# Performance work log

Hardware: AMD Instinct MI355X
Metric: run time of the kernel (lower is better)

The kernel has to match this reference:

```python
import jax, jax.numpy as jnp
import numpy as np

N = 50000      # num nodes
E = 600000     # num edges (avg degree 12)
IN = 256       # in_feats
H = 128        # h_feats
P = 2          # prop_step
LN_EPS = 1e-5


def setup_inputs() -> dict:
    key = jax.random.key(0)
    ks = jax.random.split(key, 8)
    return {
        "in_feat": jax.random.normal(ks[0], (N, IN), jnp.float32),
        "row": jax.random.randint(ks[1], (E,), 0, N),  # target node of each edge
        "col": jax.random.randint(ks[2], (E,), 0, N),  # source node of each edge
        "lin_w": jax.random.normal(ks[3], (H, IN), jnp.float32) / np.sqrt(IN).astype(np.float32),
        "lin_b": jnp.zeros((H,), jnp.float32),
        "conv_w": jax.random.normal(ks[4], (H, H), jnp.float32) / np.sqrt(H).astype(np.float32),
        "conv_b": jnp.zeros((H,), jnp.float32),
        "root_emb": jax.random.normal(ks[5], (1, H), jnp.float32) * 0.02,
        "ln_gamma": jnp.ones((P, H), jnp.float32),
        "ln_beta": jnp.zeros((P, H), jnp.float32),
    }


def _layernorm(x, g, b):
    mu = jnp.mean(x, axis=-1, keepdims=True)
    var = jnp.mean(jnp.square(x - mu), axis=-1, keepdims=True)
    return (x - mu) * jax.lax.rsqrt(var + LN_EPS) * g + b


def reference(in_feat, row, col, lin_w, lin_b, conv_w, conv_b, root_emb, ln_gamma, ln_beta):
    n = in_feat.shape[0]
    h = in_feat @ lin_w.T + lin_b                      # [N, H]

    # OGB-style degree norm with +1 trick (original edges, row = target)
    deg = jax.ops.segment_sum(jnp.ones_like(row, dtype=h.dtype), row, num_segments=n) + 1.0
    deg_inv = 1.0 / deg                                # deg >= 1, never inf

    # GCNConv symmetric norm with self loops: D^-1/2 (A+I) D^-1/2
    loop = jnp.arange(n)
    r2 = jnp.concatenate([row, loop])                  # [E+N] targets
    c2 = jnp.concatenate([col, loop])                  # [E+N] sources
    d2 = jax.ops.segment_sum(jnp.ones_like(r2, dtype=h.dtype), r2, num_segments=n)
    dis = jnp.where(d2 > 0, jax.lax.rsqrt(jnp.maximum(d2, 1.0)), 0.0)
    ew = dis[r2] * dis[c2]                             # [E+N] edge weights

    root = root_emb[0]                                 # [H]
    ori = h
    for i in range(P):
        if i != 0:
            h = h + ori                                # residual
            h = _layernorm(h, ln_gamma[i], ln_beta[i])
            h = jax.nn.relu(h)
            # dropout=0.0 -> identity
        xw = h @ conv_w.T                              # [N, H]
        h_msg = jax.ops.segment_sum(ew[:, None] * xw[c2], r2, num_segments=n) + conv_b
        root_contrib = jax.nn.relu(h + root) * deg_inv[:, None]
        h = h_msg + root_contrib
    return h
```

## Files before the change

kernel.cpp:

```cpp
#include <hip/hip_runtime.h>
#include <stdint.h>

#define NN 50000
#define EE 600000
#define INF 256
#define HF 128
#define CEB ((EE + 255) / 256)
#define GBT ((NN + 63) / 64)
#define NT0 500
#define NT1 (GBT - NT0)
#define NBCH ((NN + 255) / 256)

typedef __attribute__((ext_vector_type(8))) short short8;
typedef __attribute__((ext_vector_type(4))) float floatx4;

__device__ __forceinline__ unsigned short f32_to_bf16_rne(float x) {
    unsigned int u = __float_as_uint(x);
    unsigned int r = (u + 0x7FFFu + ((u >> 16) & 1u)) >> 16;
    return (unsigned short)r;
}
__device__ __forceinline__ float bf16_to_f32(unsigned short h) {
    return __uint_as_float(((unsigned int)h) << 16);
}
__device__ __forceinline__ float bf16lo_u32(unsigned int u) {
    return __uint_as_float(u << 16);
}
__device__ __forceinline__ float bf16hi_u32(unsigned int u) {
    return __uint_as_float(u & 0xFFFF0000u);
}
__device__ __forceinline__ void cvt_hilo8(float4 v0, float4 v1, short8& hs, short8& ls) {
    float x[8] = {v0.x, v0.y, v0.z, v0.w, v1.x, v1.y, v1.z, v1.w};
    union { short8 s; unsigned short u[8]; } H, L;
#pragma unroll
    for (int k = 0; k < 8; ++k) {
        unsigned short hi = f32_to_bf16_rne(x[k]);
        H.u[k] = hi;
        L.u[k] = f32_to_bf16_rne(x[k] - bf16_to_f32(hi));
    }
    hs = H.s;
    ls = L.s;
}

__device__ __forceinline__ void prepack_one(int idx, const float* lw, const float* cw,
                                            unsigned short* fl, unsigned short* fc) {
    const float* src; unsigned short* dst; int K, c;
    if (idx < 8192) { src = lw; dst = fl; K = INF; c = idx; }
    else            { src = cw; dst = fc; K = HF; c = idx - 8192; }
    int lane = c & 63;
    int nt = (c >> 6) & 7;
    int hl = (c >> 9) & 1;
    int kc = c >> 10;
    int rw = nt * 16 + (lane & 15);
    int koff = kc * 32 + (lane >> 4) * 8;
    const float* p = &src[(size_t)rw * K + koff];
    float4 v0 = *reinterpret_cast<const float4*>(p);
    float4 v1 = *reinterpret_cast<const float4*>(p + 4);
    short8 hs, ls;
    cvt_hilo8(v0, v1, hs, ls);
    *reinterpret_cast<short8*>(&dst[(size_t)c * 8]) = hl ? ls : hs;
}

__global__ void zero_prepack(const float* __restrict__ lw, const float* __restrict__ cw,
                             unsigned short* __restrict__ fl, unsigned short* __restrict__ fc,
                             int* __restrict__ cnt, int* __restrict__ done_ctr) {
    int g = blockIdx.x * 256 + threadIdx.x;
    if (g < 12288) prepack_one(g, lw, cw, fl, fc);
    for (int i = g; i < NN; i += 256 * 256) cnt[i] = 0;
    if (g == 0) *done_ctr = 0;
}

__global__ void scan_all(const int* __restrict__ cnt, int* __restrict__ bsum,
                         int* __restrict__ done_ctr, int* __restrict__ row_start,
                         float* __restrict__ deg_inv, float* __restrict__ dis) {
    __shared__ int sdata[256];
    __shared__ int eb[256];
    __shared__ int flag;
    int c = blockIdx.x, t = threadIdx.x;
    int i = c * 256 + t;
    int v = (i < NN) ? cnt[i] : 0;
    sdata[t] = v;
    __syncthreads();
    for (int s = 1; s < 256; s <<= 1) {
        int add = (t >= s) ? sdata[t - s] : 0;
        __syncthreads();
        sdata[t] += add;
        __syncthreads();
    }
    if (i < NN) {
        row_start[i] = sdata[t] - v;
        float d = (float)(v + 1);
        deg_inv[i] = 1.0f / d;
        dis[i] = rsqrtf(d);
    }
    if (t == 255) bsum[c] = sdata[255];
    __syncthreads();
    if (t == 0) {
        __threadfence();
        flag = (atomicAdd(done_ctr, 1) == NBCH - 1);
    }
    __syncthreads();
    if (!flag) return;
    __threadfence();
    int bv = (t < NBCH) ? bsum[t] : 0;
    sdata[t] = bv;
    __syncthreads();
    for (int s = 1; s < 256; s <<= 1) {
        int add = (t >= s) ? sdata[t - s] : 0;
        __syncthreads();
        sdata[t] += add;
        __syncthreads();
    }
    eb[t] = sdata[t] - bv;
    __syncthreads();
    for (int j = t; j < NN; j += 256) row_start[j] += eb[j >> 8];
    if (t == 0) row_start[NN] = EE;
}

template <int K, int MODE>
__device__ __forceinline__ void gemm_tile(
    int bidx,
    const float* __restrict__ Af,
    const unsigned short* __restrict__ Ahg, const unsigned short* __restrict__ Alg,
    const unsigned short* __restrict__ Wf,
    const float* __restrict__ bias,
    float* __restrict__ C, unsigned short* __restrict__ Cbf,
    const float* __restrict__ h, const float* __restrict__ deg_inv,
    const float* __restrict__ root,
    const float* __restrict__ gamma, const float* __restrict__ beta,
    unsigned short* WS, int M) {
    constexpr int NKC = K / 32;
    const int t = threadIdx.x;
    const int wave = t >> 6;
    const int lane = t & 63;
    const int lrow = lane & 15;
    const int quad = lane >> 4;
    const int bm = bidx * 64;
    int arow = bm + wave * 16 + lrow;
    if (arow >= M) arow = M - 1;

    floatx4 acc[8];
#pragma unroll
    for (int nt = 0; nt < 8; ++nt) acc[nt] = (floatx4){0.f, 0.f, 0.f, 0.f};

#pragma unroll
    for (int pp = 0; pp < NKC / 2; ++pp) {
        if (pp) __syncthreads();
        {
            const unsigned short* src = Wf + (size_t)pp * 16384 + (size_t)t * 8;
#if __has_builtin(__builtin_amdgcn_global_load_lds)
#pragma unroll
            for (int i = 0; i < 8; ++i) {
                __builtin_amdgcn_global_load_lds(
                    (const unsigned int*)(src + (size_t)i * 2048),
                    (unsigned int*)(WS + ((size_t)i * 256 + (t >> 6) * 64) * 8),
                    16, 0, 0);
            }
#else
            const uint4* s4 = reinterpret_cast<const uint4*>(Wf + (size_t)pp * 16384);
            uint4* d4 = reinterpret_cast<uint4*>(WS);
#pragma unroll
            for (int i = 0; i < 8; ++i) d4[t + 256 * i] = s4[t + 256 * i];
#endif
        }
        __syncthreads();
#pragma unroll
        for (int k2 = 0; k2 < 2; ++k2) {
            int kc = pp * 2 + k2;
            short8 afh, afl;
            if (MODE == 0) {
                const float* ap = &Af[(size_t)arow * K + kc * 32 + quad * 8];
                float4 a0 = *reinterpret_cast<const float4*>(ap);
                float4 a1 = *reinterpret_cast<const float4*>(ap + 4);
                cvt_hilo8(a0, a1, afh, afl);
            } else {
                size_t ao = (size_t)arow * K + kc * 32 + quad * 8;
                afh = *reinterpret_cast<const short8*>(&Ahg[ao]);
                afl = *reinterpret_cast<const short8*>(&Alg[ao]);
            }
            const unsigned short* wb = &WS[k2 * 8192 + lane * 8];
#pragma unroll
            for (int nt = 0; nt < 8; ++nt) {
                short8 bfh = *reinterpret_cast<const short8*>(wb + nt * 512);
                short8 bfl = *reinterpret_cast<const short8*>(wb + 4096 + nt * 512);
                acc[nt] = __builtin_amdgcn_mfma_f32_16x16x32_bf16(afh, bfh, acc[nt], 0, 0, 0);
                acc[nt] = __builtin_amdgcn_mfma_f32_16x16x32_bf16(afl, bfh, acc[nt], 0, 0, 0);
                acc[nt] = __builtin_amdgcn_mfma_f32_16x16x32_bf16(afh, bfl, acc[nt], 0, 0, 0);
            }
        }
    }

    float cb[8], rt[8], gm[8], bt[8];
#pragma unroll
    for (int nt = 0; nt < 8; ++nt) {
        int colh = nt * 16 + lrow;
        cb[nt] = bias[colh];
        if (MODE >= 1) rt[nt] = root[colh];
        if (MODE == 1) { gm[nt] = gamma[colh]; bt[nt] = beta[colh]; }
    }

#pragma unroll
    for (int r = 0; r < 4; ++r) {
        int grow = bm + wave * 16 + quad * 4 + r;
        bool ok = (grow < M);
        int gr = ok ? grow : M - 1;
        float x[8];
        if (MODE == 0) {
#pragma unroll
            for (int nt = 0; nt < 8; ++nt) x[nt] = acc[nt][r] + cb[nt];
        } else {
            float di = deg_inv[gr];
            float hv[8];
#pragma unroll
            for (int nt = 0; nt < 8; ++nt) hv[nt] = h[(size_t)gr * HF + nt * 16 + lrow];
#pragma unroll
            for (int nt = 0; nt < 8; ++nt) {
                float v = acc[nt][r] + cb[nt] + fmaxf(hv[nt] + rt[nt], 0.f) * di;
                x[nt] = (MODE == 1) ? v + hv[nt] : v;
            }
        }
        if (MODE == 1) {
            float s = 0.f;
#pragma unroll
            for (int nt = 0; nt < 8; ++nt) s += x[nt];
#pragma unroll
            for (int m = 1; m < 16; m <<= 1) s += __shfl_xor(s, m, 64);
            float mu = s * (1.0f / HF);
            float var = 0.f;
#pragma unroll
            for (int nt = 0; nt < 8; ++nt) { float d = x[nt] - mu; var += d * d; }
#pragma unroll
            for (int m = 1; m < 16; m <<= 1) var += __shfl_xor(var, m, 64);
            float rs = rsqrtf(var * (1.0f / HF) + 1e-5f);
            if (ok) {
#pragma unroll
                for (int nt = 0; nt < 8; ++nt) {
                    int colh = nt * 16 + lrow;
                    float y = fmaxf((x[nt] - mu) * rs * gm[nt] + bt[nt], 0.f);
                    C[(size_t)grow * HF + colh] = y;
                    Cbf[(size_t)grow * HF + colh] = f32_to_bf16_rne(y);
                }
            }
        } else if (MODE == 0) {
            if (ok) {
#pragma unroll
                for (int nt = 0; nt < 8; ++nt) {
                    int colh = nt * 16 + lrow;
                    C[(size_t)grow * HF + colh] = x[nt];
                    Cbf[(size_t)grow * HF + colh] = f32_to_bf16_rne(x[nt]);
                }
            }
        } else {
            if (ok) {
#pragma unroll
                for (int nt = 0; nt < 8; ++nt)
                    C[(size_t)grow * HF + nt * 16 + lrow] = x[nt];
            }
        }
    }
}

__global__ __launch_bounds__(256) void gemm0_count(
    const float* __restrict__ in_feat, const unsigned short* __restrict__ fl,
    const float* __restrict__ lin_b,
    float* __restrict__ h0, unsigned short* __restrict__ hbf,
    const int* __restrict__ row, int* __restrict__ cnt, int* __restrict__ pos) {
    __shared__ unsigned short WS[2 * 8192];
    int b = blockIdx.x;
    if (b < NT0) {
        gemm_tile<INF, 0>(b, in_feat, nullptr, nullptr, fl, lin_b,
                          h0, hbf, nullptr, nullptr, nullptr,
                          nullptr, nullptr, WS, NN);
        return;
    }
    int e = (b - NT0) * 256 + threadIdx.x;
    if (e < EE) pos[e] = atomicAdd(&cnt[row[e]], 1);
}

__global__ __launch_bounds__(256) void gemm0_fill(
    const float* __restrict__ in_feat, const unsigned short* __restrict__ fl,
    const float* __restrict__ lin_b,
    float* __restrict__ h0, unsigned short* __restrict__ hbf,
    const int* __restrict__ row, const int* __restrict__ col,
    const int* __restrict__ row_start, const int* __restrict__ pos,
    int* __restrict__ csr_col) {
    __shared__ unsigned short WS[2 * 8192];
    int b = blockIdx.x;
    if (b < NT1) {
        gemm_tile<INF, 0>(NT0 + b, in_feat, nullptr, nullptr, fl, lin_b,
                          h0, hbf, nullptr, nullptr, nullptr,
                          nullptr, nullptr, WS, NN);
        return;
    }
    int e = (b - NT1) * 256 + threadIdx.x;
    if (e < EE) {
        int p = row_start[row[e]] + pos[e];
        __builtin_nontemporal_store(col[e], &csr_col[p]);
    }
}

template <int MODE>
__global__ __launch_bounds__(256) void gemm_conv(
    const unsigned short* __restrict__ agg_hi, const unsigned short* __restrict__ agg_lo,
    const unsigned short* __restrict__ fc, const float* __restrict__ conv_b,
    float* __restrict__ C, unsigned short* __restrict__ Cbf,
    const float* __restrict__ h, const float* __restrict__ deg_inv,
    const float* __restrict__ root,
    const float* __restrict__ gamma, const float* __restrict__ beta) {
    __shared__ unsigned short WS[2 * 8192];
    gemm_tile<HF, MODE>(blockIdx.x, nullptr, agg_hi, agg_lo, fc, conv_b,
                        C, Cbf, h, deg_inv, root, gamma, beta, WS, NN);
}

__global__ void aggregate(const int* __restrict__ row_start, const int* __restrict__ csr_col,
                          const float* __restrict__ dis, const float* __restrict__ deg_inv,
                          const float* __restrict__ h, const unsigned short* __restrict__ hbf,
                          unsigned short* __restrict__ agg_hi, unsigned short* __restrict__ agg_lo,
                          int n) {
    int wid = (blockIdx.x * blockDim.x + threadIdx.x) >> 6;
    int lane = threadIdx.x & 63;
    if (wid >= n) return;
    int q = lane >> 4;
    int l16 = lane & 15;
    int s = row_start[wid];
    int e = row_start[wid + 1];
    float a0 = 0.f, a1 = 0.f, a2 = 0.f, a3 = 0.f, a4 = 0.f, a5 = 0.f, a6 = 0.f, a7 = 0.f;
    if (e - s <= 16) {
        int j0 = s + q;
        bool p0 = j0 < e, p1 = j0 + 4 < e, p2 = j0 + 8 < e, p3 = j0 + 12 < e;
        int c0 = p0 ? csr_col[j0] : 0;
        int c1 = p1 ? csr_col[j0 + 4] : 0;
        int c2 = p2 ? csr_col[j0 + 8] : 0;
        int c3 = p3 ? csr_col[j0 + 12] : 0;
        float d0 = dis[c0], d1 = dis[c1], d2 = dis[c2], d3 = dis[c3];
        uint4 z = make_uint4(0, 0, 0, 0);
        uint4 g0 = z, g1 = z, g2 = z, g3 = z;
        if (p0) g0 = *reinterpret_cast<const uint4*>(&hbf[(size_t)c0 * HF + l16 * 8]);
        if (p1) g1 = *reinterpret_cast<const uint4*>(&hbf[(size_t)c1 * HF + l16 * 8]);
        if (p2) g2 = *reinterpret_cast<const uint4*>(&hbf[(size_t)c2 * HF + l16 * 8]);
        if (p3) g3 = *reinterpret_cast<const uint4*>(&hbf[(size_t)c3 * HF + l16 * 8]);
        a0 = d0 * bf16lo_u32(g0.x) + d1 * bf16lo_u32(g1.x) + d2 * bf16lo_u32(g2.x) + d3 * bf16lo_u32(g3.x);
        a1 = d0 * bf16hi_u32(g0.x) + d1 * bf16hi_u32(g1.x) + d2 * bf16hi_u32(g2.x) + d3 * bf16hi_u32(g3.x);
        a2 = d0 * bf16lo_u32(g0.y) + d1 * bf16lo_u32(g1.y) + d2 * bf16lo_u32(g2.y) + d3 * bf16lo_u32(g3.y);
        a3 = d0 * bf16hi_u32(g0.y) + d1 * bf16hi_u32(g1.y) + d2 * bf16hi_u32(g2.y) + d3 * bf16hi_u32(g3.y);
        a4 = d0 * bf16lo_u32(g0.z) + d1 * bf16lo_u32(g1.z) + d2 * bf16lo_u32(g2.z) + d3 * bf16lo_u32(g3.z);
        a5 = d0 * bf16hi_u32(g0.z) + d1 * bf16hi_u32(g1.z) + d2 * bf16hi_u32(g2.z) + d3 * bf16hi_u32(g3.z);
        a6 = d0 * bf16lo_u32(g0.w) + d1 * bf16lo_u32(g1.w) + d2 * bf16lo_u32(g2.w) + d3 * bf16lo_u32(g3.w);
        a7 = d0 * bf16hi_u32(g0.w) + d1 * bf16hi_u32(g1.w) + d2 * bf16hi_u32(g2.w) + d3 * bf16hi_u32(g3.w);
    } else {
        float b0 = 0.f, b1 = 0.f, b2 = 0.f, b3 = 0.f, b4 = 0.f, b5 = 0.f, b6 = 0.f, b7 = 0.f;
        int j = s + q;
        for (; j + 4 < e; j += 8) {
            int c0 = csr_col[j];
            int c1 = csr_col[j + 4];
            float d0 = dis[c0];
            float d1 = dis[c1];
            uint4 h0 = *reinterpret_cast<const uint4*>(&hbf[(size_t)c0 * HF + l16 * 8]);
            uint4 h1 = *reinterpret_cast<const uint4*>(&hbf[(size_t)c1 * HF + l16 * 8]);
            a0 = fmaf(d0, bf16lo_u32(h0.x), a0); a1 = fmaf(d0, bf16hi_u32(h0.x), a1);
            a2 = fmaf(d0, bf16lo_u32(h0.y), a2); a3 = fmaf(d0, bf16hi_u32(h0.y), a3);
            a4 = fmaf(d0, bf16lo_u32(h0.z), a4); a5 = fmaf(d0, bf16hi_u32(h0.z), a5);
            a6 = fmaf(d0, bf16lo_u32(h0.w), a6); a7 = fmaf(d0, bf16hi_u32(h0.w), a7);
            b0 = fmaf(d1, bf16lo_u32(h1.x), b0); b1 = fmaf(d1, bf16hi_u32(h1.x), b1);
            b2 = fmaf(d1, bf16lo_u32(h1.y), b2); b3 = fmaf(d1, bf16hi_u32(h1.y), b3);
            b4 = fmaf(d1, bf16lo_u32(h1.z), b4); b5 = fmaf(d1, bf16hi_u32(h1.z), b5);
            b6 = fmaf(d1, bf16lo_u32(h1.w), b6); b7 = fmaf(d1, bf16hi_u32(h1.w), b7);
        }
        if (j < e) {
            int c0 = csr_col[j];
            float d0 = dis[c0];
            uint4 h0 = *reinterpret_cast<const uint4*>(&hbf[(size_t)c0 * HF + l16 * 8]);
            a0 = fmaf(d0, bf16lo_u32(h0.x), a0); a1 = fmaf(d0, bf16hi_u32(h0.x), a1);
            a2 = fmaf(d0, bf16lo_u32(h0.y), a2); a3 = fmaf(d0, bf16hi_u32(h0.y), a3);
            a4 = fmaf(d0, bf16lo_u32(h0.z), a4); a5 = fmaf(d0, bf16hi_u32(h0.z), a5);
            a6 = fmaf(d0, bf16lo_u32(h0.w), a6); a7 = fmaf(d0, bf16hi_u32(h0.w), a7);
        }
        a0 += b0; a1 += b1; a2 += b2; a3 += b3;
        a4 += b4; a5 += b5; a6 += b6; a7 += b7;
    }
#pragma unroll
    for (int m = 16; m < 64; m <<= 1) {
        a0 += __shfl_xor(a0, m, 64);
        a1 += __shfl_xor(a1, m, 64);
        a2 += __shfl_xor(a2, m, 64);
        a3 += __shfl_xor(a3, m, 64);
        a4 += __shfl_xor(a4, m, 64);
        a5 += __shfl_xor(a5, m, 64);
        a6 += __shfl_xor(a6, m, 64);
        a7 += __shfl_xor(a7, m, 64);
    }
    if (q == 0) {
        float dn = dis[wid];
        float di = deg_inv[wid];
        float4 hA = *reinterpret_cast<const float4*>(&h[(size_t)wid * HF + l16 * 8]);
        float4 hB = *reinterpret_cast<const float4*>(&h[(size_t)wid * HF + l16 * 8 + 4]);
        float o[8];
        o[0] = fmaf(dn, a0, di * hA.x);
        o[1] = fmaf(dn, a1, di * hA.y);
        o[2] = fmaf(dn, a2, di * hA.z);
        o[3] = fmaf(dn, a3, di * hA.w);
        o[4] = fmaf(dn, a4, di * hB.x);
        o[5] = fmaf(dn, a5, di * hB.y);
        o[6] = fmaf(dn, a6, di * hB.z);
        o[7] = fmaf(dn, a7, di * hB.w);
        unsigned short hi[8], lo[8];
#pragma unroll
        for (int k = 0; k < 8; ++k) {
            hi[k] = f32_to_bf16_rne(o[k]);
            lo[k] = f32_to_bf16_rne(o[k] - bf16_to_f32(hi[k]));
        }
        uint4 hp, lp;
        hp.x = (unsigned)hi[0] | ((unsigned)hi[1] << 16);
        hp.y = (unsigned)hi[2] | ((unsigned)hi[3] << 16);
        hp.z = (unsigned)hi[4] | ((unsigned)hi[5] << 16);
        hp.w = (unsigned)hi[6] | ((unsigned)hi[7] << 16);
        lp.x = (unsigned)lo[0] | ((unsigned)lo[1] << 16);
        lp.y = (unsigned)lo[2] | ((unsigned)lo[3] << 16);
        lp.z = (unsigned)lo[4] | ((unsigned)lo[5] << 16);
        lp.w = (unsigned)lo[6] | ((unsigned)lo[7] << 16);
        *reinterpret_cast<uint4*>(&agg_hi[(size_t)wid * HF + l16 * 8]) = hp;
        *reinterpret_cast<uint4*>(&agg_lo[(size_t)wid * HF + l16 * 8]) = lp;
    }
}

extern "C" void kernel_launch(void* const* d_in, const int* in_sizes, int n_in,
                              void* d_out, int out_size, void* d_ws, size_t ws_size,
                              hipStream_t stream) {
    const int N = NN;
    const float* in_feat = (const float*)d_in[0];
    const int* row = (const int*)d_in[1];
    const int* col = (const int*)d_in[2];
    const float* lin_w = (const float*)d_in[3];
    const float* lin_b = (const float*)d_in[4];
    const float* conv_w = (const float*)d_in[5];
    const float* conv_b = (const float*)d_in[6];
    const float* root_emb = (const float*)d_in[7];
    const float* ln_gamma = (const float*)d_in[8];
    const float* ln_beta = (const float*)d_in[9];
    float* out = (float*)d_out;

    float* ws = (float*)d_ws;
    size_t o = 0;
    float* deg_inv = ws + o; o += N;
    float* dis = ws + o; o += N;
    int* cnt = (int*)(ws + o); o += N;
    int* row_start = (int*)(ws + o); o += N + 4;
    int* pos = (int*)(ws + o); o += EE;
    int* bsum = (int*)(ws + o); o += 256;
    int* done_ctr = (int*)(ws + o); o += 4;
    int* csr_col = (int*)(ws + o); o += EE;
    unsigned short* fl = (unsigned short*)(ws + o); o += 32768;
    unsigned short* fc = (unsigned short*)(ws + o); o += 16384;
    float* h0 = ws + o; o += (size_t)N * HF;
    unsigned short* hbf = (unsigned short*)(ws + o); o += (size_t)N * HF / 2;
    unsigned short* agg_hi = (unsigned short*)(ws + o); o += (size_t)N * HF / 2;
    unsigned short* agg_lo = (unsigned short*)(ws + o); o += (size_t)N * HF / 2;

    const int WB = (N + 3) / 4;

    zero_prepack<<<256, 256, 0, stream>>>(lin_w, conv_w, fl, fc, cnt, done_ctr);
    gemm0_count<<<NT0 + CEB, 256, 0, stream>>>(in_feat, fl, lin_b, h0, hbf, row, cnt, pos);
    scan_all<<<NBCH, 256, 0, stream>>>(cnt, bsum, done_ctr, row_start, deg_inv, dis);
    gemm0_fill<<<NT1 + CEB, 256, 0, stream>>>(in_feat, fl, lin_b, h0, hbf,
                                              row, col, row_start, pos, csr_col);

    aggregate<<<WB, 256, 0, stream>>>(row_start, csr_col, dis, deg_inv, h0, hbf,
                                      agg_hi, agg_lo, N);
    gemm_conv<1><<<GBT, 256, 0, stream>>>(agg_hi, agg_lo, fc, conv_b, h0, hbf,
                                          h0, deg_inv, root_emb,
                                          ln_gamma + HF, ln_beta + HF);

    aggregate<<<WB, 256, 0, stream>>>(row_start, csr_col, dis, deg_inv, h0, hbf,
                                      agg_hi, agg_lo, N);
    gemm_conv<2><<<GBT, 256, 0, stream>>>(agg_hi, agg_lo, fc, conv_b, out, nullptr,
                                          h0, deg_inv, root_emb, nullptr, nullptr);
}
```

Before: 308.9 us.

## Reorder GCN as transform-then-aggregate and fuse epilogue into aggregation

Before, each step aggregated bf16 features into hi/lo buffers and then ran a GEMM whose epilogue did bias, root, residual and layernorm. Now each step first computes xW into hi/lo bf16 buffers and then aggregates neighbour rows of xW, applying bias, root term, residual, layernorm and ReLU inside the aggregation kernel. The bf16 copy of h is dropped and the first GEMM runs fully in gemm0_count, while the conv GEMM for step one is fused with the CSR fill. This shifts the gather from h to xw_hi and gives the GEMM a lighter epilogue, but adds extra hi/lo reads per node and leaves all of gemm0 in one launch instead of split across two.

```diff
diff --git a/kernel.cpp b/kernel.cpp
--- a/kernel.cpp
+++ b/kernel.cpp
@@ -7,8 +7,6 @@
 #define HF 128
 #define CEB ((EE + 255) / 256)
 #define GBT ((NN + 63) / 64)
-#define NT0 500
-#define NT1 (GBT - NT0)
 #define NBCH ((NN + 255) / 256)
 
 typedef __attribute__((ext_vector_type(8))) short short8;
@@ -118,15 +116,9 @@
 
 template <int K, int MODE>
 __device__ __forceinline__ void gemm_tile(
-    int bidx,
-    const float* __restrict__ Af,
-    const unsigned short* __restrict__ Ahg, const unsigned short* __restrict__ Alg,
-    const unsigned short* __restrict__ Wf,
-    const float* __restrict__ bias,
-    float* __restrict__ C, unsigned short* __restrict__ Cbf,
-    const float* __restrict__ h, const float* __restrict__ deg_inv,
-    const float* __restrict__ root,
-    const float* __restrict__ gamma, const float* __restrict__ beta,
+    int bidx, const float* __restrict__ Af, const unsigned short* __restrict__ Wf,
+    const float* __restrict__ bias, float* __restrict__ Cf,
+    unsigned short* __restrict__ Chi, unsigned short* __restrict__ Clo,
     unsigned short* WS, int M) {
     constexpr int NKC = K / 32;
     const int t = threadIdx.x;
@@ -166,17 +158,11 @@
 #pragma unroll
         for (int k2 = 0; k2 < 2; ++k2) {
             int kc = pp * 2 + k2;
+            const float* ap = &Af[(size_t)arow * K + kc * 32 + quad * 8];
+            float4 a0 = *reinterpret_cast<const float4*>(ap);
+            float4 a1 = *reinterpret_cast<const float4*>(ap + 4);
             short8 afh, afl;
-            if (MODE == 0) {
-                const float* ap = &Af[(size_t)arow * K + kc * 32 + quad * 8];
-                float4 a0 = *reinterpret_cast<const float4*>(ap);
-                float4 a1 = *reinterpret_cast<const float4*>(ap + 4);
-                cvt_hilo8(a0, a1, afh, afl);
-            } else {
-                size_t ao = (size_t)arow * K + kc * 32 + quad * 8;
-                afh = *reinterpret_cast<const short8*>(&Ahg[ao]);
-                afl = *reinterpret_cast<const short8*>(&Alg[ao]);
-            }
+            cvt_hilo8(a0, a1, afh, afl);
             const unsigned short* wb = &WS[k2 * 8192 + lane * 8];
 #pragma unroll
             for (int nt = 0; nt < 8; ++nt) {
@@ -189,133 +175,79 @@
         }
     }
 
-    float cb[8], rt[8], gm[8], bt[8];
-#pragma unroll
-    for (int nt = 0; nt < 8; ++nt) {
-        int colh = nt * 16 + lrow;
-        cb[nt] = bias[colh];
-        if (MODE >= 1) rt[nt] = root[colh];
-        if (MODE == 1) { gm[nt] = gamma[colh]; bt[nt] = beta[colh]; }
+    float cb[8];
+    if (MODE == 0) {
+#pragma unroll
+        for (int nt = 0; nt < 8; ++nt) cb[nt] = bias[nt * 16 + lrow];
     }
 
 #pragma unroll
     for (int r = 0; r < 4; ++r) {
         int grow = bm + wave * 16 + quad * 4 + r;
-        bool ok = (grow < M);
-        int gr = ok ? grow : M - 1;
-        float x[8];
-        if (MODE == 0) {
-#pragma unroll
-            for (int nt = 0; nt < 8; ++nt) x[nt] = acc[nt][r] + cb[nt];
-        } else {
-            float di = deg_inv[gr];
-            float hv[8];
-#pragma unroll
-            for (int nt = 0; nt < 8; ++nt) hv[nt] = h[(size_t)gr * HF + nt * 16 + lrow];
-#pragma unroll
-            for (int nt = 0; nt < 8; ++nt) {
-                float v = acc[nt][r] + cb[nt] + fmaxf(hv[nt] + rt[nt], 0.f) * di;
-                x[nt] = (MODE == 1) ? v + hv[nt] : v;
+        if (grow >= M) continue;
+#pragma unroll
+        for (int nt = 0; nt < 8; ++nt) {
+            int colh = nt * 16 + lrow;
+            if (MODE == 0) {
+                Cf[(size_t)grow * HF + colh] = acc[nt][r] + cb[nt];
+            } else {
+                float x = acc[nt][r];
+                unsigned short hi = f32_to_bf16_rne(x);
+                Chi[(size_t)grow * HF + colh] = hi;
+                Clo[(size_t)grow * HF + colh] = f32_to_bf16_rne(x - bf16_to_f32(hi));
             }
         }
-        if (MODE == 1) {
-            float s = 0.f;
-#pragma unroll
-            for (int nt = 0; nt < 8; ++nt) s += x[nt];
-#pragma unroll
-            for (int m = 1; m < 16; m <<= 1) s += __shfl_xor(s, m, 64);
-            float mu = s * (1.0f / HF);
-            float var = 0.f;
-#pragma unroll
-            for (int nt = 0; nt < 8; ++nt) { float d = x[nt] - mu; var += d * d; }
-#pragma unroll
-            for (int m = 1; m < 16; m <<= 1) var += __shfl_xor(var, m, 64);
-            float rs = rsqrtf(var * (1.0f / HF) + 1e-5f);
-            if (ok) {
-#pragma unroll
-                for (int nt = 0; nt < 8; ++nt) {
-                    int colh = nt * 16 + lrow;
-                    float y = fmaxf((x[nt] - mu) * rs * gm[nt] + bt[nt], 0.f);
-                    C[(size_t)grow * HF + colh] = y;
-                    Cbf[(size_t)grow * HF + colh] = f32_to_bf16_rne(y);
-                }
-            }
-        } else if (MODE == 0) {
-            if (ok) {
-#pragma unroll
-                for (int nt = 0; nt < 8; ++nt) {
-                    int colh = nt * 16 + lrow;
-                    C[(size_t)grow * HF + colh] = x[nt];
-                    Cbf[(size_t)grow * HF + colh] = f32_to_bf16_rne(x[nt]);
-                }
-            }
-        } else {
-            if (ok) {
-#pragma unroll
-                for (int nt = 0; nt < 8; ++nt)
-                    C[(size_t)grow * HF + nt * 16 + lrow] = x[nt];
-            }
-        }
     }
 }
 
 __global__ __launch_bounds__(256) void gemm0_count(
     const float* __restrict__ in_feat, const unsigned short* __restrict__ fl,
-    const float* __restrict__ lin_b,
-    float* __restrict__ h0, unsigned short* __restrict__ hbf,
+    const float* __restrict__ lin_b, float* __restrict__ h0,
     const int* __restrict__ row, int* __restrict__ cnt, int* __restrict__ pos) {
     __shared__ unsigned short WS[2 * 8192];
     int b = blockIdx.x;
-    if (b < NT0) {
-        gemm_tile<INF, 0>(b, in_feat, nullptr, nullptr, fl, lin_b,
-                          h0, hbf, nullptr, nullptr, nullptr,
-                          nullptr, nullptr, WS, NN);
+    if (b < GBT) {
+        gemm_tile<INF, 0>(b, in_feat, fl, lin_b, h0, nullptr, nullptr, WS, NN);
         return;
     }
-    int e = (b - NT0) * 256 + threadIdx.x;
+    int e = (b - GBT) * 256 + threadIdx.x;
     if (e < EE) pos[e] = atomicAdd(&cnt[row[e]], 1);
 }
 
-__global__ __launch_bounds__(256) void gemm0_fill(
-    const float* __restrict__ in_feat, const unsigned short* __restrict__ fl,
-    const float* __restrict__ lin_b,
-    float* __restrict__ h0, unsigned short* __restrict__ hbf,
+__global__ __launch_bounds__(256) void xw_fill(
+    const float* __restrict__ h, const unsigned short* __restrict__ fc,
+    unsigned short* __restrict__ xw_hi, unsigned short* __restrict__ xw_lo,
     const int* __restrict__ row, const int* __restrict__ col,
     const int* __restrict__ row_start, const int* __restrict__ pos,
     int* __restrict__ csr_col) {
     __shared__ unsigned short WS[2 * 8192];
     int b = blockIdx.x;
-    if (b < NT1) {
-        gemm_tile<INF, 0>(NT0 + b, in_feat, nullptr, nullptr, fl, lin_b,
-                          h0, hbf, nullptr, nullptr, nullptr,
-                          nullptr, nullptr, WS, NN);
+    if (b < GBT) {
+        gemm_tile<HF, 1>(b, h, fc, nullptr, nullptr, xw_hi, xw_lo, WS, NN);
         return;
     }
-    int e = (b - NT1) * 256 + threadIdx.x;
+    int e = (b - GBT) * 256 + threadIdx.x;
     if (e < EE) {
         int p = row_start[row[e]] + pos[e];
         __builtin_nontemporal_store(col[e], &csr_col[p]);
     }
 }
 
-template <int MODE>
-__global__ __launch_bounds__(256) void gemm_conv(
-    const unsigned short* __restrict__ agg_hi, const unsigned short* __restrict__ agg_lo,
-    const unsigned short* __restrict__ fc, const float* __restrict__ conv_b,
-    float* __restrict__ C, unsigned short* __restrict__ Cbf,
-    const float* __restrict__ h, const float* __restrict__ deg_inv,
-    const float* __restrict__ root,
-    const float* __restrict__ gamma, const float* __restrict__ beta) {
+__global__ __launch_bounds__(256) void xw_only(
+    const float* __restrict__ h, const unsigned short* __restrict__ fc,
+    unsigned short* __restrict__ xw_hi, unsigned short* __restrict__ xw_lo) {
     __shared__ unsigned short WS[2 * 8192];
-    gemm_tile<HF, MODE>(blockIdx.x, nullptr, agg_hi, agg_lo, fc, conv_b,
-                        C, Cbf, h, deg_inv, root, gamma, beta, WS, NN);
-}
-
-__global__ void aggregate(const int* __restrict__ row_start, const int* __restrict__ csr_col,
-                          const float* __restrict__ dis, const float* __restrict__ deg_inv,
-                          const float* __restrict__ h, const unsigned short* __restrict__ hbf,
-                          unsigned short* __restrict__ agg_hi, unsigned short* __restrict__ agg_lo,
-                          int n) {
+    gemm_tile<HF, 1>(blockIdx.x, h, fc, nullptr, nullptr, xw_hi, xw_lo, WS, NN);
+}
+
+template <int STEP>
+__global__ void agg_ep(const int* __restrict__ row_start, const int* __restrict__ csr_col,
+                       const float* __restrict__ dis, const float* __restrict__ deg_inv,
+                       const unsigned short* __restrict__ xw_hi,
+                       const unsigned short* __restrict__ xw_lo,
+                       const float* __restrict__ conv_b, const float* __restrict__ root,
+                       const float* __restrict__ gamma, const float* __restrict__ beta,
+                       float* __restrict__ h, float* __restrict__ outp, int n) {
     int wid = (blockIdx.x * blockDim.x + threadIdx.x) >> 6;
     int lane = threadIdx.x & 63;
     if (wid >= n) return;
@@ -334,10 +266,10 @@
         float d0 = dis[c0], d1 = dis[c1], d2 = dis[c2], d3 = dis[c3];
         uint4 z = make_uint4(0, 0, 0, 0);
         uint4 g0 = z, g1 = z, g2 = z, g3 = z;
-        if (p0) g0 = *reinterpret_cast<const uint4*>(&hbf[(size_t)c0 * HF + l16 * 8]);
-        if (p1) g1 = *reinterpret_cast<const uint4*>(&hbf[(size_t)c1 * HF + l16 * 8]);
-        if (p2) g2 = *reinterpret_cast<const uint4*>(&hbf[(size_t)c2 * HF + l16 * 8]);
-        if (p3) g3 = *reinterpret_cast<const uint4*>(&hbf[(size_t)c3 * HF + l16 * 8]);
+        if (p0) g0 = *reinterpret_cast<const uint4*>(&xw_hi[(size_t)c0 * HF + l16 * 8]);
+        if (p1) g1 = *reinterpret_cast<const uint4*>(&xw_hi[(size_t)c1 * HF + l16 * 8]);
+        if (p2) g2 = *reinterpret_cast<const uint4*>(&xw_hi[(size_t)c2 * HF + l16 * 8]);
+        if (p3) g3 = *reinterpret_cast<const uint4*>(&xw_hi[(size_t)c3 * HF + l16 * 8]);
         a0 = d0 * bf16lo_u32(g0.x) + d1 * bf16lo_u32(g1.x) + d2 * bf16lo_u32(g2.x) + d3 * bf16lo_u32(g3.x);
         a1 = d0 * bf16hi_u32(g0.x) + d1 * bf16hi_u32(g1.x) + d2 * bf16hi_u32(g2.x) + d3 * bf16hi_u32(g3.x);
         a2 = d0 * bf16lo_u32(g0.y) + d1 * bf16lo_u32(g1.y) + d2 * bf16lo_u32(g2.y) + d3 * bf16lo_u32(g3.y);
@@ -354,25 +286,25 @@
             int c1 = csr_col[j + 4];
             float d0 = dis[c0];
             float d1 = dis[c1];
-            uint4 h0 = *reinterpret_cast<const uint4*>(&hbf[(size_t)c0 * HF + l16 * 8]);
-            uint4 h1 = *reinterpret_cast<const uint4*>(&hbf[(size_t)c1 * HF + l16 * 8]);
-            a0 = fmaf(d0, bf16lo_u32(h0.x), a0); a1 = fmaf(d0, bf16hi_u32(h0.x), a1);
-            a2 = fmaf(d0, bf16lo_u32(h0.y), a2); a3 = fmaf(d0, bf16hi_u32(h0.y), a3);
-            a4 = fmaf(d0, bf16lo_u32(h0.z), a4); a5 = fmaf(d0, bf16hi_u32(h0.z), a5);
-            a6 = fmaf(d0, bf16lo_u32(h0.w), a6); a7 = fmaf(d0, bf16hi_u32(h0.w), a7);
-            b0 = fmaf(d1, bf16lo_u32(h1.x), b0); b1 = fmaf(d1, bf16hi_u32(h1.x), b1);
-            b2 = fmaf(d1, bf16lo_u32(h1.y), b2); b3 = fmaf(d1, bf16hi_u32(h1.y), b3);
-            b4 = fmaf(d1, bf16lo_u32(h1.z), b4); b5 = fmaf(d1, bf16hi_u32(h1.z), b5);
-            b6 = fmaf(d1, bf16lo_u32(h1.w), b6); b7 = fmaf(d1, bf16hi_u32(h1.w), b7);
+            uint4 h0v = *reinterpret_cast<const uint4*>(&xw_hi[(size_t)c0 * HF + l16 * 8]);
+            uint4 h1v = *reinterpret_cast<const uint4*>(&xw_hi[(size_t)c1 * HF + l16 * 8]);
+            a0 = fmaf(d0, bf16lo_u32(h0v.x), a0); a1 = fmaf(d0, bf16hi_u32(h0v.x), a1);
+            a2 = fmaf(d0, bf16lo_u32(h0v.y), a2); a3 = fmaf(d0, bf16hi_u32(h0v.y), a3);
+            a4 = fmaf(d0, bf16lo_u32(h0v.z), a4); a5 = fmaf(d0, bf16hi_u32(h0v.z), a5);
+            a6 = fmaf(d0, bf16lo_u32(h0v.w), a6); a7 = fmaf(d0, bf16hi_u32(h0v.w), a7);
+            b0 = fmaf(d1, bf16lo_u32(h1v.x), b0); b1 = fmaf(d1, bf16hi_u32(h1v.x), b1);
+            b2 = fmaf(d1, bf16lo_u32(h1v.y), b2); b3 = fmaf(d1, bf16hi_u32(h1v.y), b3);
+            b4 = fmaf(d1, bf16lo_u32(h1v.z), b4); b5 = fmaf(d1, bf16hi_u32(h1v.z), b5);
+            b6 = fmaf(d1, bf16lo_u32(h1v.w), b6); b7 = fmaf(d1, bf16hi_u32(h1v.w), b7);
         }
         if (j < e) {
             int c0 = csr_col[j];
             float d0 = dis[c0];
-            uint4 h0 = *reinterpret_cast<const uint4*>(&hbf[(size_t)c0 * HF + l16 * 8]);
-            a0 = fmaf(d0, bf16lo_u32(h0.x), a0); a1 = fmaf(d0, bf16hi_u32(h0.x), a1);
-            a2 = fmaf(d0, bf16lo_u32(h0.y), a2); a3 = fmaf(d0, bf16hi_u32(h0.y), a3);
-            a4 = fmaf(d0, bf16lo_u32(h0.z), a4); a5 = fmaf(d0, bf16hi_u32(h0.z), a5);
-            a6 = fmaf(d0, bf16lo_u32(h0.w), a6); a7 = fmaf(d0, bf16hi_u32(h0.w), a7);
+            uint4 h0v = *reinterpret_cast<const uint4*>(&xw_hi[(size_t)c0 * HF + l16 * 8]);
+            a0 = fmaf(d0, bf16lo_u32(h0v.x), a0); a1 = fmaf(d0, bf16hi_u32(h0v.x), a1);
+            a2 = fmaf(d0, bf16lo_u32(h0v.y), a2); a3 = fmaf(d0, bf16hi_u32(h0v.y), a3);
+            a4 = fmaf(d0, bf16lo_u32(h0v.z), a4); a5 = fmaf(d0, bf16hi_u32(h0v.z), a5);
+            a6 = fmaf(d0, bf16lo_u32(h0v.w), a6); a7 = fmaf(d0, bf16hi_u32(h0v.w), a7);
         }
         a0 += b0; a1 += b1; a2 += b2; a3 += b3;
         a4 += b4; a5 += b5; a6 += b6; a7 += b7;
@@ -388,37 +320,58 @@
         a6 += __shfl_xor(a6, m, 64);
         a7 += __shfl_xor(a7, m, 64);
     }
-    if (q == 0) {
-        float dn = dis[wid];
-        float di = deg_inv[wid];
-        float4 hA = *reinterpret_cast<const float4*>(&h[(size_t)wid * HF + l16 * 8]);
-        float4 hB = *reinterpret_cast<const float4*>(&h[(size_t)wid * HF + l16 * 8 + 4]);
-        float o[8];
-        o[0] = fmaf(dn, a0, di * hA.x);
-        o[1] = fmaf(dn, a1, di * hA.y);
-        o[2] = fmaf(dn, a2, di * hA.z);
-        o[3] = fmaf(dn, a3, di * hA.w);
-        o[4] = fmaf(dn, a4, di * hB.x);
-        o[5] = fmaf(dn, a5, di * hB.y);
-        o[6] = fmaf(dn, a6, di * hB.z);
-        o[7] = fmaf(dn, a7, di * hB.w);
-        unsigned short hi[8], lo[8];
-#pragma unroll
-        for (int k = 0; k < 8; ++k) {
-            hi[k] = f32_to_bf16_rne(o[k]);
-            lo[k] = f32_to_bf16_rne(o[k] - bf16_to_f32(hi[k]));
-        }
-        uint4 hp, lp;
-        hp.x = (unsigned)hi[0] | ((unsigned)hi[1] << 16);
-        hp.y = (unsigned)hi[2] | ((unsigned)hi[3] << 16);
-        hp.z = (unsigned)hi[4] | ((unsigned)hi[5] << 16);
-        hp.w = (unsigned)hi[6] | ((unsigned)hi[7] << 16);
-        lp.x = (unsigned)lo[0] | ((unsigned)lo[1] << 16);
-        lp.y = (unsigned)lo[2] | ((unsigned)lo[3] << 16);
-        lp.z = (unsigned)lo[4] | ((unsigned)lo[5] << 16);
-        lp.w = (unsigned)lo[6] | ((unsigned)lo[7] << 16);
-        *reinterpret_cast<uint4*>(&agg_hi[(size_t)wid * HF + l16 * 8]) = hp;
-        *reinterpret_cast<uint4*>(&agg_lo[(size_t)wid * HF + l16 * 8]) = lp;
+    if (q != 0) return;
+    float av[8] = {a0, a1, a2, a3, a4, a5, a6, a7};
+    int f = l16 * 8;
+    float dn = dis[wid];
+    float di = deg_inv[wid];
+    uint4 xh = *reinterpret_cast<const uint4*>(&xw_hi[(size_t)wid * HF + f]);
+    uint4 xl = *reinterpret_cast<const uint4*>(&xw_lo[(size_t)wid * HF + f]);
+    float sf[8];
+    sf[0] = bf16lo_u32(xh.x) + bf16lo_u32(xl.x);
+    sf[1] = bf16hi_u32(xh.x) + bf16hi_u32(xl.x);
+    sf[2] = bf16lo_u32(xh.y) + bf16lo_u32(xl.y);
+    sf[3] = bf16hi_u32(xh.y) + bf16hi_u32(xl.y);
+    sf[4] = bf16lo_u32(xh.z) + bf16lo_u32(xl.z);
+    sf[5] = bf16hi_u32(xh.z) + bf16hi_u32(xl.z);
+    sf[6] = bf16lo_u32(xh.w) + bf16lo_u32(xl.w);
+    sf[7] = bf16hi_u32(xh.w) + bf16hi_u32(xl.w);
+    float4 hA = *reinterpret_cast<const float4*>(&h[(size_t)wid * HF + f]);
+    float4 hB = *reinterpret_cast<const float4*>(&h[(size_t)wid * HF + f + 4]);
+    float hv[8] = {hA.x, hA.y, hA.z, hA.w, hB.x, hB.y, hB.z, hB.w};
+    float v[8];
+#pragma unroll
+    for (int k = 0; k < 8; ++k) {
+        float msg = fmaf(dn, av[k], di * sf[k]) + conv_b[f + k];
+        v[k] = msg + fmaxf(hv[k] + root[f + k], 0.f) * di;
+    }
+    if (STEP == 0) {
+        float x[8];
+        float ssum = 0.f;
+#pragma unroll
+        for (int k = 0; k < 8; ++k) { x[k] = v[k] + hv[k]; ssum += x[k]; }
+#pragma unroll
+        for (int m = 1; m < 16; m <<= 1) ssum += __shfl_xor(ssum, m, 64);
+        float mu = ssum * (1.0f / HF);
+        float var = 0.f;
+#pragma unroll
+        for (int k = 0; k < 8; ++k) { float d = x[k] - mu; var += d * d; }
+#pragma unroll
+        for (int m = 1; m < 16; m <<= 1) var += __shfl_xor(var, m, 64);
+        float rs = rsqrtf(var * (1.0f / HF) + 1e-5f);
+        float y[8];
+#pragma unroll
+        for (int k = 0; k < 8; ++k)
+            y[k] = fmaxf((x[k] - mu) * rs * gamma[f + k] + beta[f + k], 0.f);
+        *reinterpret_cast<float4*>(&h[(size_t)wid * HF + f]) =
+            make_float4(y[0], y[1], y[2], y[3]);
+        *reinterpret_cast<float4*>(&h[(size_t)wid * HF + f + 4]) =
+            make_float4(y[4], y[5], y[6], y[7]);
+    } else {
+        *reinterpret_cast<float4*>(&outp[(size_t)wid * HF + f]) =
+            make_float4(v[0], v[1], v[2], v[3]);
+        *reinterpret_cast<float4*>(&outp[(size_t)wid * HF + f + 4]) =
+            make_float4(v[4], v[5], v[6], v[7]);
     }
 }
 
@@ -451,26 +404,21 @@
     unsigned short* fl = (unsigned short*)(ws + o); o += 32768;
     unsigned short* fc = (unsigned short*)(ws + o); o += 16384;
     float* h0 = ws + o; o += (size_t)N * HF;
-    unsigned short* hbf = (unsigned short*)(ws + o); o += (size_t)N * HF / 2;
-    unsigned short* agg_hi = (unsigned short*)(ws + o); o += (size_t)N * HF / 2;
-    unsigned short* agg_lo = (unsigned short*)(ws + o); o += (size_t)N * HF / 2;
+    unsigned short* xw_hi = (unsigned short*)(ws + o); o += (size_t)N * HF / 2;
+    unsigned short* xw_lo = (unsigned short*)(ws + o); o += (size_t)N * HF / 2;
 
     const int WB = (N + 3) / 4;
 
     zero_prepack<<<256, 256, 0, stream>>>(lin_w, conv_w, fl, fc, cnt, done_ctr);
-    gemm0_count<<<NT0 + CEB, 256, 0, stream>>>(in_feat, fl, lin_b, h0, hbf, row, cnt, pos);
+    gemm0_count<<<GBT + CEB, 256, 0, stream>>>(in_feat, fl, lin_b, h0, row, cnt, pos);
     scan_all<<<NBCH, 256, 0, stream>>>(cnt, bsum, done_ctr, row_start, deg_inv, dis);
-    gemm0_fill<<<NT1 + CEB, 256, 0, stream>>>(in_feat, fl, lin_b, h0, hbf,
-                                              row, col, row_start, pos, csr_col);
-
-    aggregate<<<WB, 256, 0, stream>>>(row_start, csr_col, dis, deg_inv, h0, hbf,
-                                      agg_hi, agg_lo, N);
-    gemm_conv<1><<<GBT, 256, 0, stream>>>(agg_hi, agg_lo, fc, conv_b, h0, hbf,
-                                          h0, deg_inv, root_emb,
-                                          ln_gamma + HF, ln_beta + HF);
-
-    aggregate<<<WB, 256, 0, stream>>>(row_start, csr_col, dis, deg_inv, h0, hbf,
-                                      agg_hi, agg_lo, N);
-    gemm_conv<2><<<GBT, 256, 0, stream>>>(agg_hi, agg_lo, fc, conv_b, out, nullptr,
-                                          h0, deg_inv, root_emb, nullptr, nullptr);
-}
+    xw_fill<<<GBT + CEB, 256, 0, stream>>>(h0, fc, xw_hi, xw_lo,
+                                           row, col, row_start, pos, csr_col);
+    agg_ep<0><<<WB, 256, 0, stream>>>(row_start, csr_col, dis, deg_inv, xw_hi, xw_lo,
+                                      conv_b, root_emb, ln_gamma + HF, ln_beta + HF,
+                                      h0, nullptr, N);
+    xw_only<<<GBT, 256, 0, stream>>>(h0, fc, xw_hi, xw_lo);
+    agg_ep<1><<<WB, 256, 0, stream>>>(row_start, csr_col, dis, deg_inv, xw_hi, xw_lo,
+                                      conv_b, root_emb, nullptr, nullptr,
+                                      h0, out, N);
+}
```

Result: faster. 292.0 us (-5.5%).
